# Kernel tuning notes

Hardware: AMD Instinct MI355X
Metric: run time of the kernel (lower is better)

The kernel has to match this reference:

```python
import jax, jax.numpy as jnp
import numpy as np

EMBED = 1024
HEADS = 16
HEAD_DIM = EMBED // HEADS


def setup_inputs() -> dict:
    key = jax.random.key(0)
    ks = jax.random.split(key, 9)
    s = 1.0 / np.sqrt(EMBED)
    return {
        "embeddings": jax.random.normal(ks[0], (4, 2048, EMBED), dtype=jnp.float32),
        "wq": jax.random.uniform(ks[1], (EMBED, EMBED), jnp.float32, -s, s),
        "bq": jax.random.uniform(ks[2], (EMBED,), jnp.float32, -s, s),
        "wk": jax.random.uniform(ks[3], (EMBED, EMBED), jnp.float32, -s, s),
        "bk": jax.random.uniform(ks[4], (EMBED,), jnp.float32, -s, s),
        "wv": jax.random.uniform(ks[5], (EMBED, EMBED), jnp.float32, -s, s),
        "bv": jax.random.uniform(ks[6], (EMBED,), jnp.float32, -s, s),
        "wo": jax.random.uniform(ks[7], (EMBED, EMBED), jnp.float32, -s, s),
        "bo": jax.random.uniform(ks[8], (EMBED,), jnp.float32, -s, s),
    }


def reference(embeddings, wq, bq, wk, bk, wv, bv, wo, bo):
    b, s, _ = embeddings.shape
    # Projections: x @ W^T + b (torch nn.Linear convention)
    q = (embeddings @ wq.T + bq).reshape(b, s, HEADS, HEAD_DIM)
    k = (embeddings @ wk.T + bk).reshape(b, s, HEADS, HEAD_DIM)
    v = (embeddings @ wv.T + bv).reshape(b, s, HEADS, HEAD_DIM)
    scale = 1.0 / np.sqrt(HEAD_DIM).astype(np.float32)
    # scores: [b, h, s, s]
    scores = jnp.einsum("bqhd,bkhd->bhqk", q, k) * scale
    probs = jax.nn.softmax(scores, axis=-1)
    attn = jnp.einsum("bhqk,bkhd->bqhd", probs, v).reshape(b, s, EMBED)
    return attn @ wo.T + bo
```

## Files before the change

### kernel.cpp

```cpp
#include <hip/hip_runtime.h>
#include <hip/hip_bf16.h>
#include <math.h>

using bf16x8 = __attribute__((ext_vector_type(8))) short;
using f32x4  = __attribute__((ext_vector_type(4))) float;
using f32x16 = __attribute__((ext_vector_type(16))) float;
using i32x4  = __attribute__((ext_vector_type(4))) int;

#define MFMA_BF16(a, b, c) __builtin_amdgcn_mfma_f32_16x16x32_bf16((a), (b), (c), 0, 0, 0)
#define MFMA32(a, b, c)    __builtin_amdgcn_mfma_f32_32x32x16_bf16((a), (b), (c), 0, 0, 0)

__device__ __forceinline__ float bf2f(short s) {
    union { unsigned u; float f; } v;
    v.u = ((unsigned)(unsigned short)s) << 16;
    return v.f;
}
__device__ __forceinline__ short f2bf(float f) {
    union { float f; unsigned u; } v; v.f = f;
    unsigned r = v.u + 0x7FFF + ((v.u >> 16) & 1);
    return (short)(r >> 16);
}
__device__ __forceinline__ int cvtpk_bf16(float lo, float hi) {
    int r;
    asm("v_cvt_pk_bf16_f32 %0, %1, %2" : "=v"(r) : "v"(lo), "v"(hi));
    return r;
}
__device__ __forceinline__ void permswap(int &a, int &b) {
#if __has_builtin(__builtin_amdgcn_permlane32_swap)
    typedef unsigned u32x2v __attribute__((ext_vector_type(2)));
    u32x2v r = __builtin_amdgcn_permlane32_swap((unsigned)a, (unsigned)b, false, false);
    a = (int)r[0]; b = (int)r[1];
#else
    asm volatile("v_permlane32_swap_b32 %0, %1" : "+v"(a), "+v"(b));
#endif
}
__device__ __forceinline__ float fexp2(float x) {
#if __has_builtin(__builtin_amdgcn_exp2f)
    return __builtin_amdgcn_exp2f(x);
#else
    return exp2f(x);
#endif
}

__device__ __forceinline__ void gload_lds16(const void* g, void* l) {
    __builtin_amdgcn_global_load_lds(
        (const __attribute__((address_space(1))) void*)g,
        (__attribute__((address_space(3))) void*)l, 16, 0, 0);
}

__global__ void detect_dtype(const unsigned short* __restrict__ emb, int* flag) {
    __shared__ int tot;
    if (threadIdx.x == 0) tot = 0;
    __syncthreads();
    int c = 0;
    for (int i = 0; i < 64; i++) {
        unsigned short v = emb[2 * (threadIdx.x * 64 + i)];
        unsigned e = (v >> 7) & 0xFF;
        if (v == 0 || v == 0x8000u || (e >= 97 && e <= 137)) c++;
    }
    atomicAdd(&tot, c);
    __syncthreads();
    if (threadIdx.x == 0) *flag = (tot > 8192) ? 1 : 0;
}

__global__ void convert8(const void* __restrict__ src, short* __restrict__ dst,
                         int n8, const int* __restrict__ flag) {
    int i = blockIdx.x * 256 + threadIdx.x;
    if (i >= n8) return;
    if (*flag) {
        ((bf16x8*)dst)[i] = ((const bf16x8*)src)[i];
    } else {
        const float* f = (const float*)src + (size_t)i * 8;
        bf16x8 o;
#pragma unroll
        for (int j = 0; j < 8; j++) o[j] = f2bf(f[j]);
        ((bf16x8*)dst)[i] = o;
    }
}

__global__ void convert_all(
    const void* __restrict__ w0, const void* __restrict__ w1,
    const void* __restrict__ w2, const void* __restrict__ w3,
    const void* __restrict__ b0, const void* __restrict__ b1,
    const void* __restrict__ b2, const void* __restrict__ b3,
    short* dw0, short* dw1, short* dw2, short* dw3,
    short* db0, short* db1, short* db2, short* db3,
    const int* __restrict__ flag)
{
    int i = blockIdx.x * 256 + threadIdx.x;
    const void* src; short* dst; int idx;
    if (i < 524288) {
        int w = i >> 17; idx = i & 131071;
        src = (w == 0) ? w0 : (w == 1) ? w1 : (w == 2) ? w2 : w3;
        dst = (w == 0) ? dw0 : (w == 1) ? dw1 : (w == 2) ? dw2 : dw3;
    } else {
        int j = i - 524288; int b = j >> 7; idx = j & 127;
        src = (b == 0) ? b0 : (b == 1) ? b1 : (b == 2) ? b2 : b3;
        dst = (b == 0) ? db0 : (b == 1) ? db1 : (b == 2) ? db2 : db3;
    }
    if (*flag) {
        ((bf16x8*)dst)[idx] = ((const bf16x8*)src)[idx];
    } else {
        const float* f = (const float*)src + (size_t)idx * 8;
        bf16x8 o;
#pragma unroll
        for (int j = 0; j < 8; j++) o[j] = f2bf(f[j]);
        ((bf16x8*)dst)[idx] = o;
    }
}

__global__ __launch_bounds__(256) void gemm128(
    const short* __restrict__ A,
    const short* __restrict__ B0, const short* __restrict__ B1,
    const short* __restrict__ B2,
    const short* __restrict__ bias0, const short* __restrict__ bias1,
    const short* __restrict__ bias2,
    void* __restrict__ C0, void* __restrict__ C1, void* __restrict__ C2,
    float s0, float s1, float s2,
    int mode0, int mode1, int mode2,
    const int* __restrict__ flag)
{
    constexpr int M = 8192, N = 1024, Kd = 1024, BK = 32;
    __shared__ __align__(16) short As[2][128 * BK];
    __shared__ __align__(16) short Bs[2][128 * BK];

    const int z = blockIdx.z;
    const short* B    = (z == 0) ? B0    : (z == 1) ? B1    : B2;
    const short* bias = (z == 0) ? bias0 : (z == 1) ? bias1 : bias2;
    void*  C     = (z == 0) ? C0 : (z == 1) ? C1 : C2;
    float  scale = (z == 0) ? s0 : (z == 1) ? s1 : s2;
    int    mode  = (z == 0) ? mode0 : (z == 1) ? mode1 : mode2;

    const int tid  = threadIdx.x;
    const int lane = tid & 63;
    const int wave = tid >> 6;
    const int lr   = lane & 15;
    const int quad = lane >> 4;

    const int bid = blockIdx.x;
    const int swz = ((bid & 7) << 6) | (bid >> 3);
    const int m0 = (swz >> 3) * 128;
    const int n0 = (swz & 7) * 128;
    const int wm = (wave >> 1) * 64;
    const int wn = (wave & 1) * 64;

    const int srow = lane >> 2;
    const int scol = (((lane & 3) ^ ((lane >> 3) & 3)) * 8);
    const int rchunk = (quad ^ ((lr >> 1) & 3)) * 8;

    int fl = 1;
    if (mode == 2) fl = *flag;

    f32x4 acc[4][4];
#pragma unroll
    for (int i = 0; i < 4; i++)
#pragma unroll
        for (int j = 0; j < 4; j++) acc[i][j] = (f32x4){0.f, 0.f, 0.f, 0.f};

    auto stage = [&](int bufi, int k) {
#pragma unroll
        for (int t = 0; t < 2; t++) {
            const int r = wave * 32 + t * 16;
            gload_lds16(A + (size_t)(m0 + r + srow) * Kd + k + scol,
                        &As[bufi][r * BK]);
            gload_lds16(B + (size_t)(n0 + r + srow) * Kd + k + scol,
                        &Bs[bufi][r * BK]);
        }
    };

    stage(0, 0);
    for (int k0 = 0; k0 < Kd; k0 += BK) {
        const int cur = (k0 >> 5) & 1;
        stage(cur ^ 1, (k0 + BK) & (Kd - 1));
        asm volatile("s_waitcnt vmcnt(4)" ::: "memory");
        __builtin_amdgcn_s_barrier();
        __builtin_amdgcn_sched_barrier(0);

        bf16x8 a[4], b[4];
#pragma unroll
        for (int i = 0; i < 4; i++)
            a[i] = *(const bf16x8*)(&As[cur][(wm + i * 16 + lr) * BK + rchunk]);
#pragma unroll
        for (int j = 0; j < 4; j++)
            b[j] = *(const bf16x8*)(&Bs[cur][(wn + j * 16 + lr) * BK + rchunk]);
#pragma unroll
        for (int i = 0; i < 4; i++)
#pragma unroll
            for (int j = 0; j < 4; j++)
                acc[i][j] = MFMA_BF16(a[i], b[j], acc[i][j]);

        asm volatile("s_waitcnt lgkmcnt(0)" ::: "memory");
        __builtin_amdgcn_sched_barrier(0);
        __builtin_amdgcn_s_barrier();
    }

#pragma unroll
    for (int j = 0; j < 4; j++) {
        const int col = n0 + wn + j * 16 + lr;
        const float bv = bf2f(bias[col]);
#pragma unroll
        for (int i = 0; i < 4; i++) {
#pragma unroll
            for (int r = 0; r < 4; r++) {
                const int row = m0 + wm + i * 16 + quad * 4 + r;
                const float v = (acc[i][j][r] + bv) * scale;
                if (mode == 1)      ((short*)C)[(size_t)col * M + row] = f2bf(v);
                else if (mode == 0) ((short*)C)[(size_t)row * N + col] = f2bf(v);
                else {
                    if (fl) ((short*)C)[(size_t)row * N + col] = f2bf(v);
                    else    ((float*)C)[(size_t)row * N + col] = v;
                }
            }
        }
    }
}

__global__ __launch_bounds__(256) void attn_kernel(
    const short* Q, const short* __restrict__ K,
    const short* __restrict__ Vt, short* Aout)
{
    __shared__ __align__(16) short lds[2][2][64][64];

    const int tid  = threadIdx.x;
    const int lane = tid & 63;
    const int wave = tid >> 6;
    const int l31  = lane & 31;
    const int hi   = lane >> 5;
    const int xr   = l31 & 7;

    const int qt = blockIdx.x;
    const int bh = blockIdx.y;
    const int b  = bh >> 4, h = bh & 15;
    const int q0 = b * 2048 + qt * 128 + wave * 32;
    const int c0 = h * 64;

    const int sr = lane >> 3;
    const int sc = ((lane & 7) ^ sr) * 8;
    const int sarr = wave >> 1;

    const short* Kb = K  + (size_t)(b * 2048) * 1024 + c0;
    const short* Vb = Vt + (size_t)c0 * 8192 + b * 2048;

    bf16x8 qf[4];
#pragma unroll
    for (int slot = 0; slot < 4; slot++)
        qf[slot] = *(const bf16x8*)(Q + (size_t)(q0 + l31) * 1024 + c0 + slot * 16 + hi * 8);

    auto stage = [&](int bufi, int kt) {
#pragma unroll
        for (int t = 0; t < 4; t++) {
            const int r0 = ((wave & 1) * 4 + t) * 8;
            short* dst = &lds[bufi][sarr][r0][0];
            if (sarr == 0)
                gload_lds16(Kb + (size_t)(kt + r0 + sr) * 1024 + sc, dst);
            else
                gload_lds16(Vb + (size_t)(r0 + sr) * 8192 + kt + sc, dst);
        }
    };

    float l_run = 0.f;
    f32x16 o[2];
#pragma unroll
    for (int dblk = 0; dblk < 2; dblk++)
#pragma unroll
        for (int r = 0; r < 16; r++) o[dblk][r] = 0.f;

    stage(0, 0);
    for (int kt = 0; kt < 2048; kt += 64) {
        const int cur = (kt >> 6) & 1;
        stage(cur ^ 1, (kt + 64) & 2047);
        asm volatile("s_waitcnt vmcnt(4)" ::: "memory");
        __builtin_amdgcn_s_barrier();
        __builtin_amdgcn_sched_barrier(0);

        f32x16 st[2];
#pragma unroll
        for (int blk = 0; blk < 2; blk++)
#pragma unroll
            for (int r = 0; r < 16; r++) st[blk][r] = 0.f;

#pragma unroll
        for (int blk = 0; blk < 2; blk++)
#pragma unroll
            for (int slot = 0; slot < 4; slot++) {
                bf16x8 kf = *(const bf16x8*)
                    &lds[cur][0][blk * 32 + l31][(((slot << 1) | hi) ^ xr) * 8];
                st[blk] = MFMA32(kf, qf[slot], st[blk]);
            }

        float rs = 0.f;
#pragma unroll
        for (int blk = 0; blk < 2; blk++)
#pragma unroll
            for (int r = 0; r < 16; r++) {
                float p = fexp2(st[blk][r]);
                st[blk][r] = p;
                rs += p;
            }
        l_run += rs;

#pragma unroll
        for (int ks = 0; ks < 4; ks++) {
            const int blk = ks >> 1;
            const int rb  = (ks & 1) * 8;
            int A0 = cvtpk_bf16(st[blk][rb + 0], st[blk][rb + 1]);
            int A1 = cvtpk_bf16(st[blk][rb + 2], st[blk][rb + 3]);
            int B0 = cvtpk_bf16(st[blk][rb + 4], st[blk][rb + 5]);
            int B1 = cvtpk_bf16(st[blk][rb + 6], st[blk][rb + 7]);
            permswap(A0, B0);
            permswap(A1, B1);
            i32x4 paw; paw[0] = A0; paw[1] = A1; paw[2] = B0; paw[3] = B1;
            const bf16x8 pf = *(const bf16x8*)&paw;
#pragma unroll
            for (int dblk = 0; dblk < 2; dblk++) {
                bf16x8 vf = *(const bf16x8*)
                    &lds[cur][1][dblk * 32 + l31][(((ks << 1) | hi) ^ xr) * 8];
                o[dblk] = MFMA32(pf, vf, o[dblk]);
            }
        }

        asm volatile("s_waitcnt lgkmcnt(0)" ::: "memory");
        __builtin_amdgcn_sched_barrier(0);
        __builtin_amdgcn_s_barrier();
    }

    float l_tot = l_run + __shfl_xor(l_run, 32);
#pragma unroll
    for (int r = 0; r < 16; r++) {
        const int qrow = (r & 3) + 8 * (r >> 2) + 4 * hi;
        const float inv = 1.f / __shfl(l_tot, qrow);
#pragma unroll
        for (int dblk = 0; dblk < 2; dblk++)
            Aout[(size_t)(q0 + qrow) * 1024 + c0 + dblk * 32 + l31] =
                f2bf(o[dblk][r] * inv);
    }
}

extern "C" void kernel_launch(void* const* d_in, const int* in_sizes, int n_in,
                              void* d_out, int out_size, void* d_ws, size_t ws_size,
                              hipStream_t stream)
{
    const size_t MB = (size_t)1024 * 1024;
    char* ws = (char*)d_ws;

    int*   flagp = (int*)ws;
    short* embC  = (short*)(ws + 1 * MB);
    short* wC[4] = { (short*)(ws + 17 * MB), (short*)(ws + 19 * MB),
                     (short*)(ws + 21 * MB), (short*)(ws + 23 * MB) };
    short* bC[4] = { (short*)(ws + 25 * MB), (short*)(ws + 25 * MB + 4096),
                     (short*)(ws + 25 * MB + 8192), (short*)(ws + 25 * MB + 12288) };

    short *Qb, *Kb, *Vt, *Ab;
    if (ws_size >= 90 * MB) {
        Qb = (short*)(ws + 26 * MB);
        Kb = (short*)(ws + 42 * MB);
        Vt = (short*)(ws + 58 * MB);
        Ab = (short*)(ws + 74 * MB);
    } else {
        Qb = (short*)(ws + 26 * MB);
        Kb = (short*)d_out;
        Vt = (short*)(ws + 42 * MB);
        Ab = Qb;
    }

    detect_dtype<<<1, 256, 0, stream>>>((const unsigned short*)d_in[0], flagp);

    convert8<<<4096, 256, 0, stream>>>(d_in[0], embC, 1048576, flagp);
    convert_all<<<2050, 256, 0, stream>>>(
        d_in[1], d_in[3], d_in[5], d_in[7],
        d_in[2], d_in[4], d_in[6], d_in[8],
        wC[0], wC[1], wC[2], wC[3],
        bC[0], bC[1], bC[2], bC[3], flagp);

    dim3 blk(256);
    gemm128<<<dim3(512, 1, 3), blk, 0, stream>>>(
        embC, wC[0], wC[1], wC[2], bC[0], bC[1], bC[2],
        Qb, Kb, Vt, 0.18033688011112042f, 1.0f, 1.0f, 0, 0, 1, nullptr);

    attn_kernel<<<dim3(16, 64), blk, 0, stream>>>(Qb, Kb, Vt, Ab);

    gemm128<<<dim3(512, 1, 1), blk, 0, stream>>>(
        Ab, wC[3], nullptr, nullptr, bC[3], nullptr, nullptr,
        d_out, nullptr, nullptr, 1.0f, 0.f, 0.f, 2, 0, 0, flagp);
}
```

Measured before the change: 325.0 us.

## Vectorize transposed GEMM stores, compute softmax row sums via MFMA, retune attention swizzle

The mode-1 GEMM epilogue now packs four bf16 values into one 8-byte store instead of four scalar stores. The attention kernel drops the per-lane exp summation and cross-lane shuffles, accumulating row sums by multiplying P against an all-ones matrix with an extra MFMA per k-step. It also changes the LDS XOR swizzle to reduce bank conflicts and adds a launch_bounds occupancy hint of 4 blocks. The extra MFMA adds matrix work in exchange for fewer VALU adds and shuffles, and the occupancy hint may limit registers.

```diff
diff --git a/kernel.cpp b/kernel.cpp
--- a/kernel.cpp
+++ b/kernel.cpp
@@ -6,6 +6,7 @@
 using f32x4  = __attribute__((ext_vector_type(4))) float;
 using f32x16 = __attribute__((ext_vector_type(16))) float;
 using i32x4  = __attribute__((ext_vector_type(4))) int;
+using i32x2  = __attribute__((ext_vector_type(2))) int;
 
 #define MFMA_BF16(a, b, c) __builtin_amdgcn_mfma_f32_16x16x32_bf16((a), (b), (c), 0, 0, 0)
 #define MFMA32(a, b, c)    __builtin_amdgcn_mfma_f32_32x32x16_bf16((a), (b), (c), 0, 0, 0)
@@ -194,28 +195,47 @@
         __builtin_amdgcn_s_barrier();
     }
 
-#pragma unroll
-    for (int j = 0; j < 4; j++) {
-        const int col = n0 + wn + j * 16 + lr;
-        const float bv = bf2f(bias[col]);
-#pragma unroll
-        for (int i = 0; i < 4; i++) {
-#pragma unroll
-            for (int r = 0; r < 4; r++) {
-                const int row = m0 + wm + i * 16 + quad * 4 + r;
-                const float v = (acc[i][j][r] + bv) * scale;
-                if (mode == 1)      ((short*)C)[(size_t)col * M + row] = f2bf(v);
-                else if (mode == 0) ((short*)C)[(size_t)row * N + col] = f2bf(v);
-                else {
-                    if (fl) ((short*)C)[(size_t)row * N + col] = f2bf(v);
-                    else    ((float*)C)[(size_t)row * N + col] = v;
+    if (mode == 1) {
+#pragma unroll
+        for (int j = 0; j < 4; j++) {
+            const int col = n0 + wn + j * 16 + lr;
+            const float bv = bf2f(bias[col]);
+#pragma unroll
+            for (int i = 0; i < 4; i++) {
+                const int row = m0 + wm + i * 16 + quad * 4;
+                const float v0 = (acc[i][j][0] + bv) * scale;
+                const float v1 = (acc[i][j][1] + bv) * scale;
+                const float v2 = (acc[i][j][2] + bv) * scale;
+                const float v3 = (acc[i][j][3] + bv) * scale;
+                i32x2 dd;
+                dd[0] = cvtpk_bf16(v0, v1);
+                dd[1] = cvtpk_bf16(v2, v3);
+                *(i32x2*)((short*)C + (size_t)col * M + row) = dd;
+            }
+        }
+    } else {
+#pragma unroll
+        for (int j = 0; j < 4; j++) {
+            const int col = n0 + wn + j * 16 + lr;
+            const float bv = bf2f(bias[col]);
+#pragma unroll
+            for (int i = 0; i < 4; i++) {
+#pragma unroll
+                for (int r = 0; r < 4; r++) {
+                    const int row = m0 + wm + i * 16 + quad * 4 + r;
+                    const float v = (acc[i][j][r] + bv) * scale;
+                    if (mode == 0) ((short*)C)[(size_t)row * N + col] = f2bf(v);
+                    else {
+                        if (fl) ((short*)C)[(size_t)row * N + col] = f2bf(v);
+                        else    ((float*)C)[(size_t)row * N + col] = v;
+                    }
                 }
             }
         }
     }
 }
 
-__global__ __launch_bounds__(256) void attn_kernel(
+__global__ __launch_bounds__(256, 4) void attn_kernel(
     const short* Q, const short* __restrict__ K,
     const short* __restrict__ Vt, short* Aout)
 {
@@ -226,7 +246,7 @@
     const int wave = tid >> 6;
     const int l31  = lane & 31;
     const int hi   = lane >> 5;
-    const int xr   = l31 & 7;
+    const int xr   = (l31 & 7) ^ ((l31 >> 3) & 3);
 
     const int qt = blockIdx.x;
     const int bh = blockIdx.y;
@@ -234,8 +254,8 @@
     const int q0 = b * 2048 + qt * 128 + wave * 32;
     const int c0 = h * 64;
 
-    const int sr = lane >> 3;
-    const int sc = ((lane & 7) ^ sr) * 8;
+    const int sr  = lane >> 3;
+    const int scb = (lane & 7) ^ sr;
     const int sarr = wave >> 1;
 
     const short* Kb = K  + (size_t)(b * 2048) * 1024 + c0;
@@ -250,6 +270,7 @@
 #pragma unroll
         for (int t = 0; t < 4; t++) {
             const int r0 = ((wave & 1) * 4 + t) * 8;
+            const int sc = (scb ^ t) * 8;
             short* dst = &lds[bufi][sarr][r0][0];
             if (sarr == 0)
                 gload_lds16(Kb + (size_t)(kt + r0 + sr) * 1024 + sc, dst);
@@ -258,12 +279,13 @@
         }
     };
 
-    float l_run = 0.f;
-    f32x16 o[2];
-#pragma unroll
-    for (int dblk = 0; dblk < 2; dblk++)
-#pragma unroll
-        for (int r = 0; r < 16; r++) o[dblk][r] = 0.f;
+    bf16x8 onesf;
+#pragma unroll
+    for (int j = 0; j < 8; j++) onesf[j] = (short)0x3F80;
+
+    f32x16 o[2], l_acc;
+#pragma unroll
+    for (int r = 0; r < 16; r++) { o[0][r] = 0.f; o[1][r] = 0.f; l_acc[r] = 0.f; }
 
     stage(0, 0);
     for (int kt = 0; kt < 2048; kt += 64) {
@@ -275,29 +297,22 @@
 
         f32x16 st[2];
 #pragma unroll
-        for (int blk = 0; blk < 2; blk++)
+        for (int blk = 0; blk < 2; blk++) {
 #pragma unroll
             for (int r = 0; r < 16; r++) st[blk][r] = 0.f;
-
-#pragma unroll
-        for (int blk = 0; blk < 2; blk++)
 #pragma unroll
             for (int slot = 0; slot < 4; slot++) {
                 bf16x8 kf = *(const bf16x8*)
                     &lds[cur][0][blk * 32 + l31][(((slot << 1) | hi) ^ xr) * 8];
                 st[blk] = MFMA32(kf, qf[slot], st[blk]);
             }
-
-        float rs = 0.f;
+        }
+
 #pragma unroll
         for (int blk = 0; blk < 2; blk++)
 #pragma unroll
-            for (int r = 0; r < 16; r++) {
-                float p = fexp2(st[blk][r]);
-                st[blk][r] = p;
-                rs += p;
-            }
-        l_run += rs;
+            for (int r = 0; r < 16; r++)
+                st[blk][r] = fexp2(st[blk][r]);
 
 #pragma unroll
         for (int ks = 0; ks < 4; ks++) {
@@ -311,6 +326,7 @@
             permswap(A1, B1);
             i32x4 paw; paw[0] = A0; paw[1] = A1; paw[2] = B0; paw[3] = B1;
             const bf16x8 pf = *(const bf16x8*)&paw;
+            l_acc = MFMA32(pf, onesf, l_acc);
 #pragma unroll
             for (int dblk = 0; dblk < 2; dblk++) {
                 bf16x8 vf = *(const bf16x8*)
@@ -324,11 +340,10 @@
         __builtin_amdgcn_s_barrier();
     }
 
-    float l_tot = l_run + __shfl_xor(l_run, 32);
 #pragma unroll
     for (int r = 0; r < 16; r++) {
         const int qrow = (r & 3) + 8 * (r >> 2) + 4 * hi;
-        const float inv = 1.f / __shfl(l_tot, qrow);
+        const float inv = 1.f / l_acc[r];
 #pragma unroll
         for (int dblk = 0; dblk < 2; dblk++)
             Aout[(size_t)(q0 + qrow) * 1024 + c0 + dblk * 32 + l31] =
```

New measurement: 359.0 us. +10.5%, slower.
